# Optimization experiments

Measured on AMD Instinct MI355X. Metric: run time of the kernel, lower is better.

Reference implementation:

```python
import jax, jax.numpy as jnp
import numpy as np

L = 2048          # seq len
DIM = 1024        # model dim
NL = 12           # num layers
VOCAB = 50257
PAD_VOCAB = 50264 # vocab padded to multiple of 8 for embedding
N = 16            # ssm state dim
K = 4             # conv kernel size
E = 2048          # d_inner = expand * dim
DTR = 64          # dt_rank = ceil(dim/16)
EPS = 1e-5


def setup_inputs() -> dict:
    key = jax.random.key(0)
    ks = jax.random.split(key, 12)
    s = 0.02
    f32 = jnp.float32
    # HiPPO-style A init: A_log = log(1..N) broadcast over channels
    A_log = jnp.log(jnp.broadcast_to(jnp.arange(1, N + 1, dtype=f32), (NL, E, N)))
    return {
        "input_ids": jax.random.randint(ks[0], (L,), 0, VOCAB),
        "embed": jax.random.normal(ks[1], (PAD_VOCAB, DIM), f32) * s,
        "in_proj_w": jax.random.normal(ks[2], (NL, 2 * E, DIM), f32) * s,
        "conv_w": jax.random.normal(ks[3], (NL, E, K), f32) * s,
        "conv_b": jnp.zeros((NL, E), f32),
        "x_proj_w": jax.random.normal(ks[4], (NL, DTR + 2 * N, E), f32) * s,
        "dt_proj_w": jax.random.normal(ks[5], (NL, E, DTR), f32) * s,
        "dt_proj_b": jax.random.normal(ks[6], (NL, E), f32) * 0.1,
        "A_log": A_log,
        "D_param": jnp.ones((NL, E), f32),
        "out_proj_w": jax.random.normal(ks[7], (NL, DIM, E), f32) * s,
        "norm_w": jnp.ones((NL, DIM), f32),
        "norm_f_w": jnp.ones((DIM,), f32),
        "head_w": jax.random.normal(ks[8], (VOCAB, DIM), f32) * s,
    }


def rmsnorm(x, w):
    # per-token RMSNorm over last axis (matches eqx.nn.RMSNorm vmapped per token)
    inv = jax.lax.rsqrt(jnp.mean(x * x, axis=-1, keepdims=True) + EPS)
    return x * inv * w


def causal_dw_conv(x, w, b):
    # x: [L, E], w: [E, K] depthwise causal conv, b: [E]
    out = jax.lax.conv_general_dilated(
        x.T[None],            # [1, E, L]
        w[:, None, :],        # [E, 1, K]
        (1,), [(K - 1, 0)],
        feature_group_count=E,
        dimension_numbers=("NCH", "OIH", "NCH"),
    )
    return out[0].T + b       # [L, E]


def mamba_block(x, in_w, cw, cb, xp_w, dt_w, dt_b, A_log, D, out_w):
    # x: [L, DIM]
    xz = x @ in_w.T                       # [L, 2E]
    xi, z = xz[:, :E], xz[:, E:]
    xc = jax.nn.silu(causal_dw_conv(xi, cw, cb))   # [L, E]
    dbc = xc @ xp_w.T                     # [L, DTR + 2N]
    dt = jax.nn.softplus(dbc[:, :DTR] @ dt_w.T + dt_b)  # [L, E]
    B = dbc[:, DTR:DTR + N]               # [L, N]
    C = dbc[:, DTR + N:]                  # [L, N]
    A = -jnp.exp(A_log)                   # [E, N]
    dA = jnp.exp(dt[:, :, None] * A)                       # [L, E, N]
    dBu = dt[:, :, None] * B[:, None, :] * xc[:, :, None]  # [L, E, N]

    def step(h, inp):
        dA_t, dBu_t = inp
        h = dA_t * h + dBu_t
        return h, h

    _, hs = jax.lax.scan(step, jnp.zeros((E, N), x.dtype), (dA, dBu))
    y = jnp.einsum("len,ln->le", hs, C) + D * xc
    y = y * jax.nn.silu(z)
    return y @ out_w.T                    # [L, DIM]


def reference(input_ids, embed, in_proj_w, conv_w, conv_b, x_proj_w,
              dt_proj_w, dt_proj_b, A_log, D_param, out_proj_w,
              norm_w, norm_f_w, head_w):
    x = embed[input_ids]                  # [L, DIM]
    res = None
    for i in range(NL):
        res = x + res if res is not None else x
        h = rmsnorm(res, norm_w[i])
        x = mamba_block(h, in_proj_w[i], conv_w[i], conv_b[i], x_proj_w[i],
                        dt_proj_w[i], dt_proj_b[i], A_log[i], D_param[i],
                        out_proj_w[i])
    res = x + res
    x = rmsnorm(res, norm_f_w)
    return x @ head_w.T                   # [L, VOCAB]
```

## Files before the change

### kernel.cpp

```cpp
#include <hip/hip_runtime.h>
#include <math.h>

#define LSEQ 2048
#define DMODEL 1024
#define NLAYER 12
#define NVOCAB 50257
#define NPADV 50304
#define EDIM 2048
#define NST 16
#define DTRANK 64
#define EPSV 1e-5f
#define NCHUNK 64
#define TCHUNK 32

typedef __attribute__((ext_vector_type(4))) float float4v;
typedef __attribute__((ext_vector_type(8))) short short8v;
typedef __attribute__((ext_vector_type(4))) unsigned short ushort4v;
typedef unsigned short u16;

__device__ __forceinline__ u16 f2bf(float f) {
    union { float f; unsigned int u; } v; v.f = f;
    unsigned int r = v.u + 0x7FFFu + ((v.u >> 16) & 1u);
    return (u16)(r >> 16);
}

__device__ __forceinline__ ushort4v cvt4(float4 a) {
    ushort4v r; r[0] = f2bf(a.x); r[1] = f2bf(a.y); r[2] = f2bf(a.z); r[3] = f2bf(a.w);
    return r;
}

__device__ __forceinline__ short8v pack8(float4 a, float4 b) {
    short8v r;
    r[0] = (short)f2bf(a.x); r[1] = (short)f2bf(a.y); r[2] = (short)f2bf(a.z); r[3] = (short)f2bf(a.w);
    r[4] = (short)f2bf(b.x); r[5] = (short)f2bf(b.y); r[6] = (short)f2bf(b.z); r[7] = (short)f2bf(b.w);
    return r;
}

__device__ __forceinline__ float4v mfma_bf16(short8v a, short8v b, float4v c) {
    return __builtin_amdgcn_mfma_f32_16x16x32_bf16(a, b, c, 0, 0, 0);
}

__device__ __forceinline__ void gload_lds16(const void* g, void* l) {
    __builtin_amdgcn_global_load_lds(
        (const __attribute__((address_space(1))) unsigned int*)g,
        (__attribute__((address_space(3))) unsigned int*)l,
        16, 0, 0);
}

__global__ __launch_bounds__(256) void k_embed(const int* __restrict__ ids,
                                               const float* __restrict__ emb,
                                               float* __restrict__ res) {
    const int t = blockIdx.x;
    const int row = ids[t];
    ((float4*)(res + (size_t)t * DMODEL))[threadIdx.x] =
        ((const float4*)(emb + (size_t)row * DMODEL))[threadIdx.x];
}

template<bool ADD>
__global__ __launch_bounds__(256) void k_addnorm(float* __restrict__ res,
                                                 const float* __restrict__ xin,
                                                 const float* __restrict__ w,
                                                 u16* __restrict__ h) {
    const int t = blockIdx.x;
    const int i = threadIdx.x;
    float4 r = ((float4*)(res + (size_t)t * DMODEL))[i];
    if (ADD) {
        float4 xv = ((const float4*)(xin + (size_t)t * DMODEL))[i];
        r.x += xv.x; r.y += xv.y; r.z += xv.z; r.w += xv.w;
        ((float4*)(res + (size_t)t * DMODEL))[i] = r;
    }
    float ss = r.x * r.x + r.y * r.y + r.z * r.z + r.w * r.w;
#pragma unroll
    for (int off = 32; off > 0; off >>= 1) ss += __shfl_xor(ss, off);
    __shared__ float part[4];
    if ((i & 63) == 0) part[i >> 6] = ss;
    __syncthreads();
    float tot = part[0] + part[1] + part[2] + part[3];
    const float inv = rsqrtf(tot * (1.f / DMODEL) + EPSV);
    float4 wv = ((const float4*)w)[i];
    float4 o;
    o.x = r.x * inv * wv.x; o.y = r.y * inv * wv.y;
    o.z = r.z * inv * wv.z; o.w = r.w * inv * wv.w;
    ((ushort4v*)(h + (size_t)t * DMODEL))[i] = cvt4(o);
}

__global__ __launch_bounds__(256) void k_cvt(const float* __restrict__ s, u16* __restrict__ d,
                                             long long n, long long ntot) {
    const long long stride = (long long)gridDim.x * 256 * 8;
    for (long long i = ((long long)blockIdx.x * 256 + threadIdx.x) * 8; i < ntot; i += stride) {
        ushort4v lo, hi;
        if (i < n) {
            float4 a = *(const float4*)(s + i);
            float4 b = *(const float4*)(s + i + 4);
            lo = cvt4(a); hi = cvt4(b);
        } else {
            lo[0] = lo[1] = lo[2] = lo[3] = 0;
            hi[0] = hi[1] = hi[2] = hi[3] = 0;
        }
        *(ushort4v*)(d + i) = lo;
        *(ushort4v*)(d + i + 4) = hi;
    }
}

__global__ __launch_bounds__(256) void k_cvt2(const float* __restrict__ sa, u16* __restrict__ da, long long na,
                                              const float* __restrict__ sb, u16* __restrict__ db, long long nb) {
    const long long tot = na + nb;
    const long long stride = (long long)gridDim.x * 256 * 8;
    for (long long i = ((long long)blockIdx.x * 256 + threadIdx.x) * 8; i < tot; i += stride) {
        const float* s; u16* d; long long o;
        if (i < na) { s = sa; d = da; o = i; } else { s = sb; d = db; o = i - na; }
        float4 a = *(const float4*)(s + o);
        float4 b = *(const float4*)(s + o + 4);
        *(ushort4v*)(d + o) = cvt4(a);
        *(ushort4v*)(d + o + 4) = cvt4(b);
    }
}

template<int MT>
__global__ __launch_bounds__(256, 4) void k_gemm128(const u16* __restrict__ A,
                                                    const u16* __restrict__ W,
                                                    float* __restrict__ C,
                                                    int N, int K, int ldc, int cpx) {
    __shared__ __align__(128) u16 lds[2][8192];
    const int tid = threadIdx.x;
    const int w = tid >> 6;
    const int lane = tid & 63;
    const int l16 = lane & 15;
    const int quad = lane >> 4;
    const int wm = (w >> 1) * 64;
    const int wn = (w & 1) * 64;
    const int bid = blockIdx.x;
    const int orig = (bid & 7) * cpx + (bid >> 3);
    const int bm = orig & (MT - 1);
    const int bn = orig / MT;
    const int row0 = bm * 128, col0 = bn * 128;

    const int scol = ((lane & 3) ^ ((lane >> 2) & 3)) * 8;
    const int lrow = lane >> 2;
    const u16* sbase[4];
#pragma unroll
    for (int c = 0; c < 4; ++c) {
        const int g = w * 4 + c;
        sbase[c] = (g < 8 ? A + (size_t)(row0 + g * 16 + lrow) * K
                          : W + (size_t)(col0 + (g - 8) * 16 + lrow) * K) + scol;
    }

    const int swz = (quad ^ (l16 & 3)) * 8;
    const int aoff = (wm + l16) * 32 + swz;
    const int boff = 4096 + (wn + l16) * 32 + swz;

    float4v acc[4][4];
#pragma unroll
    for (int i = 0; i < 4; ++i)
#pragma unroll
        for (int j = 0; j < 4; ++j)
#pragma unroll
            for (int r = 0; r < 4; ++r) acc[i][j][r] = 0.f;

    const int NT = K >> 5;

    auto stage_tile = [&](int buf, int t) {
#pragma unroll
        for (int c = 0; c < 4; ++c)
            gload_lds16(sbase[c] + t * 32, &lds[buf][(w * 4 + c) * 512]);
    };

    stage_tile(0, 0);
    stage_tile(1, 1);
    asm volatile("s_waitcnt vmcnt(4)" ::: "memory");
    __builtin_amdgcn_s_barrier();

    for (int n = 0; n < NT; ++n) {
        const u16* Ls = &lds[n & 1][0];
        short8v af[4], bf[4];
#pragma unroll
        for (int ii = 0; ii < 4; ++ii)
            af[ii] = *(const short8v*)&Ls[aoff + ii * 512];
#pragma unroll
        for (int j = 0; j < 4; ++j)
            bf[j] = *(const short8v*)&Ls[boff + j * 512];
        __builtin_amdgcn_s_barrier();
        __builtin_amdgcn_s_setprio(1);
#pragma unroll
        for (int ii = 0; ii < 4; ++ii)
#pragma unroll
            for (int j = 0; j < 4; ++j)
                acc[ii][j] = mfma_bf16(af[ii], bf[j], acc[ii][j]);
        __builtin_amdgcn_s_setprio(0);
        if (n + 2 < NT) {
            stage_tile(n & 1, n + 2);
            asm volatile("s_waitcnt vmcnt(4)" ::: "memory");
        } else if (n < NT - 1) {
            asm volatile("s_waitcnt vmcnt(0)" ::: "memory");
        }
        __builtin_amdgcn_s_barrier();
    }

#pragma unroll
    for (int i = 0; i < 4; ++i) {
        const int row = row0 + wm + i * 16 + quad * 4;
#pragma unroll
        for (int j = 0; j < 4; ++j) {
            const int col = col0 + wn + j * 16 + l16;
            if (col < N) {
#pragma unroll
                for (int r = 0; r < 4; ++r)
                    C[(size_t)(row + r) * ldc + col] = acc[i][j][r];
            }
        }
    }
}

template<int TM, int TN>
__global__ __launch_bounds__(256) void k_gemm_bf(const u16* __restrict__ A,
                                                 const u16* __restrict__ W,
                                                 float* __restrict__ C,
                                                 int N, int K, int ldc) {
    constexpr int NI = TM / 32, NJ = TN / 32, CA = TM / 64, CB = TN / 64;
    __shared__ u16 As[TM * 32];
    __shared__ u16 Bs[TN * 32];
    const int tid = threadIdx.x;
    const int lane = tid & 63;
    const int wave = tid >> 6;
    const int l16 = lane & 15;
    const int quad = lane >> 4;
    const int wm = (wave >> 1) * (TM / 2);
    const int wn = (wave & 1) * (TN / 2);
    const int srow = lane >> 2;
    const int scol = (((lane & 3) ^ ((lane >> 2) & 3))) * 8;
    const int bm = blockIdx.x, bn = blockIdx.y;

    const u16* Ab = A + ((size_t)bm * TM + srow) * K + scol;
    const u16* Wb = W + ((size_t)bn * TN + srow) * K + scol;

    const int qs = (quad ^ (l16 & 3)) * 8;

    float4v acc[NI][NJ];
#pragma unroll
    for (int i = 0; i < NI; ++i)
#pragma unroll
        for (int j = 0; j < NJ; ++j)
#pragma unroll
            for (int r = 0; r < 4; ++r) acc[i][j][r] = 0.f;

    for (int k0 = 0; k0 < K; k0 += 32) {
#pragma unroll
        for (int c = 0; c < CA; ++c) {
            const int chunk = wave * CA + c;
            gload_lds16(Ab + (size_t)chunk * 16 * K + k0, &As[chunk * 512]);
        }
#pragma unroll
        for (int c = 0; c < CB; ++c) {
            const int chunk = wave * CB + c;
            gload_lds16(Wb + (size_t)chunk * 16 * K + k0, &Bs[chunk * 512]);
        }
        __syncthreads();
        short8v af[NI], bfr[NJ];
#pragma unroll
        for (int i = 0; i < NI; ++i)
            af[i] = *(const short8v*)&As[(wm + i * 16 + l16) * 32 + qs];
#pragma unroll
        for (int j = 0; j < NJ; ++j)
            bfr[j] = *(const short8v*)&Bs[(wn + j * 16 + l16) * 32 + qs];
#pragma unroll
        for (int i = 0; i < NI; ++i)
#pragma unroll
            for (int j = 0; j < NJ; ++j)
                acc[i][j] = mfma_bf16(af[i], bfr[j], acc[i][j]);
        __syncthreads();
    }

#pragma unroll
    for (int i = 0; i < NI; ++i) {
        const int row0 = bm * TM + wm + i * 16 + quad * 4;
#pragma unroll
        for (int j = 0; j < NJ; ++j) {
            const int col = bn * TN + wn + j * 16 + l16;
            if (col < N) {
#pragma unroll
                for (int r = 0; r < 4; ++r)
                    C[(size_t)(row0 + r) * ldc + col] = acc[i][j][r];
            }
        }
    }
}

template<int EPI>
__global__ __launch_bounds__(256) void k_gemm(const float* __restrict__ A,
                                              const float* __restrict__ W,
                                              float* __restrict__ C,
                                              const float* __restrict__ bias,
                                              int N, int K, int lda, int ldw, int ldc) {
    __shared__ u16 As[128][32];
    __shared__ u16 Bs[128][32];
    const int tid = threadIdx.x;
    const int lane = tid & 63;
    const int wave = tid >> 6;
    const int l16 = lane & 15;
    const int quad = lane >> 4;
    const int wm = (wave >> 1) * 64;
    const int wn = (wave & 1) * 64;
    const int srow = tid >> 3;
    const int scol = (tid & 7) * 4;
    const int bm = blockIdx.x, bn = blockIdx.y;

    const float* Ap = A + (size_t)(bm * 128 + srow) * lda + scol;
    const int gn0 = bn * 128 + srow;

    float4 apf[4], bpf[4];
#pragma unroll
    for (int i = 0; i < 4; ++i) {
        apf[i] = *(const float4*)(Ap + (size_t)(32 * i) * lda);
        const int gn = gn0 + 32 * i;
        bpf[i] = (gn < N) ? *(const float4*)(W + (size_t)gn * ldw + scol)
                          : make_float4(0.f, 0.f, 0.f, 0.f);
    }

    float4v acc[4][4];
#pragma unroll
    for (int i = 0; i < 4; ++i)
#pragma unroll
        for (int j = 0; j < 4; ++j)
#pragma unroll
            for (int r = 0; r < 4; ++r) acc[i][j][r] = 0.f;

    int k0 = 0;
    while (true) {
#pragma unroll
        for (int i = 0; i < 4; ++i) {
            *(ushort4v*)&As[srow + 32 * i][scol] = cvt4(apf[i]);
            *(ushort4v*)&Bs[srow + 32 * i][scol] = cvt4(bpf[i]);
        }
        __syncthreads();
        k0 += 32;
        const bool more = (k0 < K);
        if (more) {
#pragma unroll
            for (int i = 0; i < 4; ++i) {
                apf[i] = *(const float4*)(Ap + (size_t)(32 * i) * lda + k0);
                const int gn = gn0 + 32 * i;
                bpf[i] = (gn < N) ? *(const float4*)(W + (size_t)gn * ldw + scol + k0)
                                  : make_float4(0.f, 0.f, 0.f, 0.f);
            }
        }
        short8v af[4], bfr[4];
#pragma unroll
        for (int i = 0; i < 4; ++i)
            af[i] = *(const short8v*)&As[wm + i * 16 + l16][quad * 8];
#pragma unroll
        for (int j = 0; j < 4; ++j)
            bfr[j] = *(const short8v*)&Bs[wn + j * 16 + l16][quad * 8];
#pragma unroll
        for (int i = 0; i < 4; ++i)
#pragma unroll
            for (int j = 0; j < 4; ++j)
                acc[i][j] = mfma_bf16(af[i], bfr[j], acc[i][j]);
        if (!more) break;
        __syncthreads();
    }

#pragma unroll
    for (int i = 0; i < 4; ++i) {
        const int row0 = bm * 128 + wm + i * 16 + quad * 4;
#pragma unroll
        for (int j = 0; j < 4; ++j) {
            const int col = bn * 128 + wn + j * 16 + l16;
            if (col < N) {
#pragma unroll
                for (int r = 0; r < 4; ++r) {
                    float v = acc[i][j][r];
                    if (EPI == 1) {
                        v += bias[col];
                        v = (v > 20.f) ? v : log1pf(__expf(v));
                    }
                    C[(size_t)(row0 + r) * ldc + col] = v;
                }
            }
        }
    }
}

__global__ __launch_bounds__(256) void k_conv(const float* __restrict__ xz,
                                              const float* __restrict__ cw,
                                              const float* __restrict__ cb,
                                              float* __restrict__ xc) {
    const int e = blockIdx.x * 256 + threadIdx.x;
    const int t0 = blockIdx.y * 8;
    const float w0 = cw[e * 4 + 0], w1 = cw[e * 4 + 1], w2 = cw[e * 4 + 2], w3 = cw[e * 4 + 3];
    const float b = cb[e];
    float xm3 = (t0 >= 3) ? xz[(size_t)(t0 - 3) * (2 * EDIM) + e] : 0.f;
    float xm2 = (t0 >= 2) ? xz[(size_t)(t0 - 2) * (2 * EDIM) + e] : 0.f;
    float xm1 = (t0 >= 1) ? xz[(size_t)(t0 - 1) * (2 * EDIM) + e] : 0.f;
#pragma unroll
    for (int s = 0; s < 8; ++s) {
        const int t = t0 + s;
        const float xt = xz[(size_t)t * (2 * EDIM) + e];
        const float v = w0 * xm3 + w1 * xm2 + w2 * xm1 + w3 * xt + b;
        xc[(size_t)t * EDIM + e] = v / (1.f + __expf(-v));
        xm3 = xm2; xm2 = xm1; xm1 = xt;
    }
}

__global__ __launch_bounds__(256) void k_xproj(const float* __restrict__ xc,
                                               const float* __restrict__ W,
                                               float* __restrict__ dbc) {
    const int tid = threadIdx.x;
    const int wave = tid >> 6, lane = tid & 63;
    const int l16 = lane & 15, quad = lane >> 4;
    const int m = blockIdx.x * 16 + l16;
    const int kb = wave * (EDIM / 4);
    float4v acc[6];
#pragma unroll
    for (int j = 0; j < 6; ++j)
#pragma unroll
        for (int r = 0; r < 4; ++r) acc[j][r] = 0.f;

    for (int ks = 0; ks < EDIM / 4; ks += 32) {
        const int k = kb + ks + quad * 8;
        const float* ap = xc + (size_t)m * EDIM + k;
        const short8v af = pack8(*(const float4*)ap, *(const float4*)(ap + 4));
#pragma unroll
        for (int j = 0; j < 6; ++j) {
            const float* wp = W + (size_t)(j * 16 + l16) * EDIM + k;
            const short8v bf = pack8(*(const float4*)wp, *(const float4*)(wp + 4));
            acc[j] = mfma_bf16(af, bf, acc[j]);
        }
    }
    __shared__ float red[4][16][96];
#pragma unroll
    for (int j = 0; j < 6; ++j)
#pragma unroll
        for (int r = 0; r < 4; ++r)
            red[wave][quad * 4 + r][j * 16 + l16] = acc[j][r];
    __syncthreads();
    for (int idx = tid; idx < 16 * 96; idx += 256) {
        const int r = idx / 96, c = idx % 96;
        const float s = red[0][r][c] + red[1][r][c] + red[2][r][c] + red[3][r][c];
        dbc[(size_t)(blockIdx.x * 16 + r) * 96 + c] = s;
    }
}

__global__ __launch_bounds__(256) void k_scanA(const float* __restrict__ dt,
                                               const float* __restrict__ xc,
                                               const float* __restrict__ dbc,
                                               const float* __restrict__ Al,
                                               float* __restrict__ hpart,
                                               float* __restrict__ sdtb) {
    const int e = blockIdx.y * 256 + threadIdx.x;
    const int c = blockIdx.x;
    float a[NST];
#pragma unroll
    for (int n = 0; n < NST; ++n) a[n] = -__expf(Al[(size_t)e * NST + n]);
    bool fast = true;
#pragma unroll
    for (int n = 0; n < NST; ++n)
        fast = fast && (fabsf(a[n] + (float)(n + 1)) < 1e-3f * (float)(n + 1));
    __align__(16) float h[NST];
#pragma unroll
    for (int n = 0; n < NST; ++n) h[n] = 0.f;
    float sdt = 0.f;
    const int t0 = c * TCHUNK;
    if (fast) {
        for (int s = 0; s < TCHUNK; ++s) {
            const int t = t0 + s;
            const float d = dt[(size_t)t * EDIM + e];
            const float x = xc[(size_t)t * EDIM + e];
            __align__(16) float Bv[NST];
#pragma unroll
            for (int q = 0; q < 4; ++q)
                *(float4*)&Bv[q * 4] = *(const float4*)&dbc[(size_t)t * 96 + 64 + q * 4];
            const float u = d * x;
            sdt += d;
            const float d1 = __expf(-d);
            float pw = 1.f;
#pragma unroll
            for (int n = 0; n < NST; ++n) { pw *= d1; h[n] = fmaf(pw, h[n], u * Bv[n]); }
        }
    } else {
        for (int s = 0; s < TCHUNK; ++s) {
            const int t = t0 + s;
            const float d = dt[(size_t)t * EDIM + e];
            const float x = xc[(size_t)t * EDIM + e];
            __align__(16) float Bv[NST];
#pragma unroll
            for (int q = 0; q < 4; ++q)
                *(float4*)&Bv[q * 4] = *(const float4*)&dbc[(size_t)t * 96 + 64 + q * 4];
            const float u = d * x;
            sdt += d;
#pragma unroll
            for (int n = 0; n < NST; ++n) h[n] = fmaf(__expf(d * a[n]), h[n], u * Bv[n]);
        }
    }
#pragma unroll
    for (int n = 0; n < NST; n += 4)
        *(float4*)&hpart[((size_t)c * EDIM + e) * NST + n] = *(float4*)&h[n];
    sdtb[(size_t)c * EDIM + e] = sdt;
}

__global__ __launch_bounds__(256) void k_scanB(float* __restrict__ hio,
                                               const float* __restrict__ sdtb,
                                               const float* __restrict__ Al) {
    const int idx = blockIdx.x * 256 + threadIdx.x;
    const int e = idx >> 4;
    const float a = -__expf(Al[idx]);
    float carry = 0.f;
    for (int c = 0; c < NCHUNK; ++c) {
        const size_t off = ((size_t)c * EDIM + e) * NST + (idx & 15);
        const float hp = hio[off];
        const float ap = __expf(a * sdtb[(size_t)c * EDIM + e]);
        hio[off] = carry;
        carry = fmaf(ap, carry, hp);
    }
}

__global__ __launch_bounds__(256) void k_scanC(const float* __restrict__ dt,
                                               const float* __restrict__ xc,
                                               const float* __restrict__ dbc,
                                               const float* __restrict__ xz,
                                               const float* __restrict__ Al,
                                               const float* __restrict__ Dl,
                                               const float* __restrict__ hin,
                                               u16* __restrict__ y) {
    const int e = blockIdx.y * 256 + threadIdx.x;
    const int c = blockIdx.x;
    float a[NST];
#pragma unroll
    for (int n = 0; n < NST; ++n) a[n] = -__expf(Al[(size_t)e * NST + n]);
    bool fast = true;
#pragma unroll
    for (int n = 0; n < NST; ++n)
        fast = fast && (fabsf(a[n] + (float)(n + 1)) < 1e-3f * (float)(n + 1));
    __align__(16) float h[NST];
#pragma unroll
    for (int n = 0; n < NST; n += 4)
        *(float4*)&h[n] = *(const float4*)&hin[((size_t)c * EDIM + e) * NST + n];
    const float Dv = Dl[e];
    const int t0 = c * TCHUNK;
    for (int s = 0; s < TCHUNK; ++s) {
        const int t = t0 + s;
        const float d = dt[(size_t)t * EDIM + e];
        const float x = xc[(size_t)t * EDIM + e];
        __align__(16) float Bv[NST], Cv[NST];
#pragma unroll
        for (int q = 0; q < 4; ++q) {
            *(float4*)&Bv[q * 4] = *(const float4*)&dbc[(size_t)t * 96 + 64 + q * 4];
            *(float4*)&Cv[q * 4] = *(const float4*)&dbc[(size_t)t * 96 + 80 + q * 4];
        }
        const float u = d * x;
        float ys = 0.f;
        if (fast) {
            const float d1 = __expf(-d);
            float pw = 1.f;
#pragma unroll
            for (int n = 0; n < NST; ++n) {
                pw *= d1;
                h[n] = fmaf(pw, h[n], u * Bv[n]);
                ys = fmaf(h[n], Cv[n], ys);
            }
        } else {
#pragma unroll
            for (int n = 0; n < NST; ++n) {
                h[n] = fmaf(__expf(d * a[n]), h[n], u * Bv[n]);
                ys = fmaf(h[n], Cv[n], ys);
            }
        }
        const float z = xz[(size_t)t * (2 * EDIM) + EDIM + e];
        const float yv = ys + Dv * x;
        y[(size_t)t * EDIM + e] = f2bf(yv * (z / (1.f + __expf(-z))));
    }
}

extern "C" void kernel_launch(void* const* d_in, const int* in_sizes, int n_in,
                              void* d_out, int out_size, void* d_ws, size_t ws_size,
                              hipStream_t stream) {
    const int*   ids   = (const int*)d_in[0];
    const float* emb   = (const float*)d_in[1];
    const float* inW   = (const float*)d_in[2];
    const float* convW = (const float*)d_in[3];
    const float* convB = (const float*)d_in[4];
    const float* xpW   = (const float*)d_in[5];
    const float* dtW   = (const float*)d_in[6];
    const float* dtB   = (const float*)d_in[7];
    const float* Alog  = (const float*)d_in[8];
    const float* Dpar  = (const float*)d_in[9];
    const float* outW  = (const float*)d_in[10];
    const float* normW = (const float*)d_in[11];
    const float* normF = (const float*)d_in[12];
    const float* headW = (const float*)d_in[13];
    float* out = (float*)d_out;

    float* ws    = (float*)d_ws;
    float* res   = ws;
    float* xzb   = res   + (size_t)LSEQ * DMODEL;
    float* xcb   = xzb   + (size_t)LSEQ * 2 * EDIM;
    float* dbcb  = xcb   + (size_t)LSEQ * EDIM;
    float* dtb   = dbcb  + (size_t)LSEQ * 96;
    float* xob   = dtb   + (size_t)LSEQ * EDIM;
    float* hpart = xob   + (size_t)LSEQ * DMODEL;
    float* sdtb  = hpart + (size_t)NCHUNK * EDIM * NST;
    u16* hbf  = (u16*)(sdtb + (size_t)NCHUNK * EDIM);
    u16* ybf  = hbf  + (size_t)LSEQ * DMODEL;
    u16* wbf  = ybf  + (size_t)LSEQ * EDIM;
    u16* wbf2 = wbf  + (size_t)2 * EDIM * DMODEL;

    k_embed<<<LSEQ, 256, 0, stream>>>(ids, emb, res);

    for (int i = 0; i < NLAYER; ++i) {
        if (i == 0)
            k_addnorm<false><<<LSEQ, 256, 0, stream>>>(res, nullptr, normW, hbf);
        else
            k_addnorm<true><<<LSEQ, 256, 0, stream>>>(res, xob, normW + (size_t)i * DMODEL, hbf);

        k_cvt2<<<4096, 256, 0, stream>>>(inW + (size_t)i * 2 * EDIM * DMODEL, wbf,
                                         (long long)2 * EDIM * DMODEL,
                                         outW + (size_t)i * DMODEL * EDIM, wbf2,
                                         (long long)DMODEL * EDIM);

        k_gemm128<16><<<dim3(512), 256, 0, stream>>>(hbf, wbf, xzb,
                2 * EDIM, DMODEL, 2 * EDIM, 64);

        k_conv<<<dim3(8, 256), 256, 0, stream>>>(xzb, convW + (size_t)i * EDIM * 4,
                convB + (size_t)i * EDIM, xcb);

        k_xproj<<<128, 256, 0, stream>>>(xcb, xpW + (size_t)i * 96 * EDIM, dbcb);

        k_gemm<1><<<dim3(16, 16), 256, 0, stream>>>(dbcb, dtW + (size_t)i * EDIM * DTRANK,
                dtb, dtB + (size_t)i * EDIM, EDIM, DTRANK, 96, DTRANK, EDIM);

        const float* Al = Alog + (size_t)i * EDIM * NST;
        k_scanA<<<dim3(NCHUNK, EDIM / 256), 256, 0, stream>>>(dtb, xcb, dbcb, Al, hpart, sdtb);
        k_scanB<<<(EDIM * NST) / 256, 256, 0, stream>>>(hpart, sdtb, Al);
        k_scanC<<<dim3(NCHUNK, EDIM / 256), 256, 0, stream>>>(dtb, xcb, dbcb, xzb, Al,
                Dpar + (size_t)i * EDIM, hpart, ybf);

        k_gemm_bf<64, 64><<<dim3(32, 16), 256, 0, stream>>>(ybf, wbf2, xob,
                DMODEL, EDIM, DMODEL);
    }

    k_addnorm<true><<<LSEQ, 256, 0, stream>>>(res, xob, normF, hbf);

    k_cvt<<<4096, 256, 0, stream>>>(headW, wbf,
            (long long)NVOCAB * DMODEL, (long long)NPADV * DMODEL);
    k_gemm128<16><<<dim3(6288), 256, 0, stream>>>(hbf, wbf, out,
            NVOCAB, DMODEL, NVOCAB, 6288 / 8);
}
```

Before: 3.158 ms.

## Pre-convert x_proj and dt_proj inputs to bf16 and reuse async GEMM

The x_proj and dt_proj weights are now converted to bf16 in the per-layer conversion kernel. The conv kernel also emits a bf16 copy of its output, and x_proj emits a bf16 copy of the dt-rank columns. This lets x_proj read bf16 directly and lets dt_proj run on the async-LDS k_gemm128 path with a fused bias+softplus epilogue, replacing the float GEMM that converted on the fly. The LDS swizzle pattern is also changed in both bf16 GEMMs, presumably to reduce bank conflicts. The cost is extra bf16 writes and a larger conversion pass.

After: 3.020 ms. -4.4%, faster.

```diff
diff --git a/kernel.cpp b/kernel.cpp
--- a/kernel.cpp
+++ b/kernel.cpp
@@ -26,13 +26,6 @@
 
 __device__ __forceinline__ ushort4v cvt4(float4 a) {
     ushort4v r; r[0] = f2bf(a.x); r[1] = f2bf(a.y); r[2] = f2bf(a.z); r[3] = f2bf(a.w);
-    return r;
-}
-
-__device__ __forceinline__ short8v pack8(float4 a, float4 b) {
-    short8v r;
-    r[0] = (short)f2bf(a.x); r[1] = (short)f2bf(a.y); r[2] = (short)f2bf(a.z); r[3] = (short)f2bf(a.w);
-    r[4] = (short)f2bf(b.x); r[5] = (short)f2bf(b.y); r[6] = (short)f2bf(b.z); r[7] = (short)f2bf(b.w);
     return r;
 }
 
@@ -102,13 +95,20 @@
     }
 }
 
-__global__ __launch_bounds__(256) void k_cvt2(const float* __restrict__ sa, u16* __restrict__ da, long long na,
-                                              const float* __restrict__ sb, u16* __restrict__ db, long long nb) {
-    const long long tot = na + nb;
+__global__ __launch_bounds__(256) void k_cvtL(const float* __restrict__ sa, u16* __restrict__ da, long long na,
+                                              const float* __restrict__ sb, u16* __restrict__ db, long long nb,
+                                              const float* __restrict__ sc, u16* __restrict__ dc, long long nc,
+                                              const float* __restrict__ sd, u16* __restrict__ dd, long long nd) {
+    const long long tot = na + nb + nc + nd;
     const long long stride = (long long)gridDim.x * 256 * 8;
     for (long long i = ((long long)blockIdx.x * 256 + threadIdx.x) * 8; i < tot; i += stride) {
-        const float* s; u16* d; long long o;
-        if (i < na) { s = sa; d = da; o = i; } else { s = sb; d = db; o = i - na; }
+        const float* s; u16* d; long long o = i;
+        if (o < na) { s = sa; d = da; }
+        else { o -= na;
+            if (o < nb) { s = sb; d = db; }
+            else { o -= nb;
+                if (o < nc) { s = sc; d = dc; }
+                else { o -= nc; s = sd; d = dd; } } }
         float4 a = *(const float4*)(s + o);
         float4 b = *(const float4*)(s + o + 4);
         *(ushort4v*)(d + o) = cvt4(a);
@@ -116,10 +116,11 @@
     }
 }
 
-template<int MT>
+template<int MT, int EPI>
 __global__ __launch_bounds__(256, 4) void k_gemm128(const u16* __restrict__ A,
                                                     const u16* __restrict__ W,
                                                     float* __restrict__ C,
+                                                    const float* __restrict__ bias,
                                                     int N, int K, int ldc, int cpx) {
     __shared__ __align__(128) u16 lds[2][8192];
     const int tid = threadIdx.x;
@@ -135,7 +136,7 @@
     const int bn = orig / MT;
     const int row0 = bm * 128, col0 = bn * 128;
 
-    const int scol = ((lane & 3) ^ ((lane >> 2) & 3)) * 8;
+    const int scol = ((lane & 3) ^ ((lane >> 3) & 3)) * 8;
     const int lrow = lane >> 2;
     const u16* sbase[4];
 #pragma unroll
@@ -145,7 +146,7 @@
                           : W + (size_t)(col0 + (g - 8) * 16 + lrow) * K) + scol;
     }
 
-    const int swz = (quad ^ (l16 & 3)) * 8;
+    const int swz = (quad ^ ((l16 >> 1) & 3)) * 8;
     const int aoff = (wm + l16) * 32 + swz;
     const int boff = 4096 + (wn + l16) * 32 + swz;
 
@@ -204,8 +205,14 @@
             const int col = col0 + wn + j * 16 + l16;
             if (col < N) {
 #pragma unroll
-                for (int r = 0; r < 4; ++r)
-                    C[(size_t)(row + r) * ldc + col] = acc[i][j][r];
+                for (int r = 0; r < 4; ++r) {
+                    float v = acc[i][j][r];
+                    if (EPI == 1) {
+                        v += bias[col];
+                        v = (v > 20.f) ? v : log1pf(__expf(v));
+                    }
+                    C[(size_t)(row + r) * ldc + col] = v;
+                }
             }
         }
     }
@@ -227,13 +234,13 @@
     const int wm = (wave >> 1) * (TM / 2);
     const int wn = (wave & 1) * (TN / 2);
     const int srow = lane >> 2;
-    const int scol = (((lane & 3) ^ ((lane >> 2) & 3))) * 8;
+    const int scol = ((lane & 3) ^ ((lane >> 3) & 3)) * 8;
     const int bm = blockIdx.x, bn = blockIdx.y;
 
     const u16* Ab = A + ((size_t)bm * TM + srow) * K + scol;
     const u16* Wb = W + ((size_t)bn * TN + srow) * K + scol;
 
-    const int qs = (quad ^ (l16 & 3)) * 8;
+    const int qs = (quad ^ ((l16 >> 1) & 3)) * 8;
 
     float4v acc[NI][NJ];
 #pragma unroll
@@ -285,105 +292,11 @@
     }
 }
 
-template<int EPI>
-__global__ __launch_bounds__(256) void k_gemm(const float* __restrict__ A,
-                                              const float* __restrict__ W,
-                                              float* __restrict__ C,
-                                              const float* __restrict__ bias,
-                                              int N, int K, int lda, int ldw, int ldc) {
-    __shared__ u16 As[128][32];
-    __shared__ u16 Bs[128][32];
-    const int tid = threadIdx.x;
-    const int lane = tid & 63;
-    const int wave = tid >> 6;
-    const int l16 = lane & 15;
-    const int quad = lane >> 4;
-    const int wm = (wave >> 1) * 64;
-    const int wn = (wave & 1) * 64;
-    const int srow = tid >> 3;
-    const int scol = (tid & 7) * 4;
-    const int bm = blockIdx.x, bn = blockIdx.y;
-
-    const float* Ap = A + (size_t)(bm * 128 + srow) * lda + scol;
-    const int gn0 = bn * 128 + srow;
-
-    float4 apf[4], bpf[4];
-#pragma unroll
-    for (int i = 0; i < 4; ++i) {
-        apf[i] = *(const float4*)(Ap + (size_t)(32 * i) * lda);
-        const int gn = gn0 + 32 * i;
-        bpf[i] = (gn < N) ? *(const float4*)(W + (size_t)gn * ldw + scol)
-                          : make_float4(0.f, 0.f, 0.f, 0.f);
-    }
-
-    float4v acc[4][4];
-#pragma unroll
-    for (int i = 0; i < 4; ++i)
-#pragma unroll
-        for (int j = 0; j < 4; ++j)
-#pragma unroll
-            for (int r = 0; r < 4; ++r) acc[i][j][r] = 0.f;
-
-    int k0 = 0;
-    while (true) {
-#pragma unroll
-        for (int i = 0; i < 4; ++i) {
-            *(ushort4v*)&As[srow + 32 * i][scol] = cvt4(apf[i]);
-            *(ushort4v*)&Bs[srow + 32 * i][scol] = cvt4(bpf[i]);
-        }
-        __syncthreads();
-        k0 += 32;
-        const bool more = (k0 < K);
-        if (more) {
-#pragma unroll
-            for (int i = 0; i < 4; ++i) {
-                apf[i] = *(const float4*)(Ap + (size_t)(32 * i) * lda + k0);
-                const int gn = gn0 + 32 * i;
-                bpf[i] = (gn < N) ? *(const float4*)(W + (size_t)gn * ldw + scol + k0)
-                                  : make_float4(0.f, 0.f, 0.f, 0.f);
-            }
-        }
-        short8v af[4], bfr[4];
-#pragma unroll
-        for (int i = 0; i < 4; ++i)
-            af[i] = *(const short8v*)&As[wm + i * 16 + l16][quad * 8];
-#pragma unroll
-        for (int j = 0; j < 4; ++j)
-            bfr[j] = *(const short8v*)&Bs[wn + j * 16 + l16][quad * 8];
-#pragma unroll
-        for (int i = 0; i < 4; ++i)
-#pragma unroll
-            for (int j = 0; j < 4; ++j)
-                acc[i][j] = mfma_bf16(af[i], bfr[j], acc[i][j]);
-        if (!more) break;
-        __syncthreads();
-    }
-
-#pragma unroll
-    for (int i = 0; i < 4; ++i) {
-        const int row0 = bm * 128 + wm + i * 16 + quad * 4;
-#pragma unroll
-        for (int j = 0; j < 4; ++j) {
-            const int col = bn * 128 + wn + j * 16 + l16;
-            if (col < N) {
-#pragma unroll
-                for (int r = 0; r < 4; ++r) {
-                    float v = acc[i][j][r];
-                    if (EPI == 1) {
-                        v += bias[col];
-                        v = (v > 20.f) ? v : log1pf(__expf(v));
-                    }
-                    C[(size_t)(row0 + r) * ldc + col] = v;
-                }
-            }
-        }
-    }
-}
-
 __global__ __launch_bounds__(256) void k_conv(const float* __restrict__ xz,
                                               const float* __restrict__ cw,
                                               const float* __restrict__ cb,
-                                              float* __restrict__ xc) {
+                                              float* __restrict__ xc,
+                                              u16* __restrict__ xc16) {
     const int e = blockIdx.x * 256 + threadIdx.x;
     const int t0 = blockIdx.y * 8;
     const float w0 = cw[e * 4 + 0], w1 = cw[e * 4 + 1], w2 = cw[e * 4 + 2], w3 = cw[e * 4 + 3];
@@ -396,14 +309,17 @@
         const int t = t0 + s;
         const float xt = xz[(size_t)t * (2 * EDIM) + e];
         const float v = w0 * xm3 + w1 * xm2 + w2 * xm1 + w3 * xt + b;
-        xc[(size_t)t * EDIM + e] = v / (1.f + __expf(-v));
+        const float sv = v / (1.f + __expf(-v));
+        xc[(size_t)t * EDIM + e] = sv;
+        xc16[(size_t)t * EDIM + e] = f2bf(sv);
         xm3 = xm2; xm2 = xm1; xm1 = xt;
     }
 }
 
-__global__ __launch_bounds__(256) void k_xproj(const float* __restrict__ xc,
-                                               const float* __restrict__ W,
-                                               float* __restrict__ dbc) {
+__global__ __launch_bounds__(256) void k_xproj(const u16* __restrict__ xc,
+                                               const u16* __restrict__ W,
+                                               float* __restrict__ dbc,
+                                               u16* __restrict__ dbc16) {
     const int tid = threadIdx.x;
     const int wave = tid >> 6, lane = tid & 63;
     const int l16 = lane & 15, quad = lane >> 4;
@@ -417,12 +333,10 @@
 
     for (int ks = 0; ks < EDIM / 4; ks += 32) {
         const int k = kb + ks + quad * 8;
-        const float* ap = xc + (size_t)m * EDIM + k;
-        const short8v af = pack8(*(const float4*)ap, *(const float4*)(ap + 4));
+        const short8v af = *(const short8v*)(xc + (size_t)m * EDIM + k);
 #pragma unroll
         for (int j = 0; j < 6; ++j) {
-            const float* wp = W + (size_t)(j * 16 + l16) * EDIM + k;
-            const short8v bf = pack8(*(const float4*)wp, *(const float4*)(wp + 4));
+            const short8v bf = *(const short8v*)(W + (size_t)(j * 16 + l16) * EDIM + k);
             acc[j] = mfma_bf16(af, bf, acc[j]);
         }
     }
@@ -436,7 +350,9 @@
     for (int idx = tid; idx < 16 * 96; idx += 256) {
         const int r = idx / 96, c = idx % 96;
         const float s = red[0][r][c] + red[1][r][c] + red[2][r][c] + red[3][r][c];
-        dbc[(size_t)(blockIdx.x * 16 + r) * 96 + c] = s;
+        const int row = blockIdx.x * 16 + r;
+        dbc[(size_t)row * 96 + c] = s;
+        if (c < 64) dbc16[(size_t)row * 64 + c] = f2bf(s);
     }
 }
 
@@ -602,6 +518,10 @@
     u16* ybf  = hbf  + (size_t)LSEQ * DMODEL;
     u16* wbf  = ybf  + (size_t)LSEQ * EDIM;
     u16* wbf2 = wbf  + (size_t)2 * EDIM * DMODEL;
+    u16* xc16  = wbf  + (size_t)12 * 1024 * 1024;
+    u16* dbc16 = xc16 + (size_t)LSEQ * EDIM;
+    u16* xpw16 = dbc16 + (size_t)LSEQ * DTRANK;
+    u16* dtw16 = xpw16 + (size_t)96 * EDIM;
 
     k_embed<<<LSEQ, 256, 0, stream>>>(ids, emb, res);
 
@@ -611,21 +531,22 @@
         else
             k_addnorm<true><<<LSEQ, 256, 0, stream>>>(res, xob, normW + (size_t)i * DMODEL, hbf);
 
-        k_cvt2<<<4096, 256, 0, stream>>>(inW + (size_t)i * 2 * EDIM * DMODEL, wbf,
-                                         (long long)2 * EDIM * DMODEL,
-                                         outW + (size_t)i * DMODEL * EDIM, wbf2,
-                                         (long long)DMODEL * EDIM);
-
-        k_gemm128<16><<<dim3(512), 256, 0, stream>>>(hbf, wbf, xzb,
+        k_cvtL<<<4096, 256, 0, stream>>>(
+            inW  + (size_t)i * 2 * EDIM * DMODEL, wbf,   (long long)2 * EDIM * DMODEL,
+            outW + (size_t)i * DMODEL * EDIM,     wbf2,  (long long)DMODEL * EDIM,
+            xpW  + (size_t)i * 96 * EDIM,         xpw16, (long long)96 * EDIM,
+            dtW  + (size_t)i * EDIM * DTRANK,     dtw16, (long long)EDIM * DTRANK);
+
+        k_gemm128<16, 0><<<dim3(512), 256, 0, stream>>>(hbf, wbf, xzb, nullptr,
                 2 * EDIM, DMODEL, 2 * EDIM, 64);
 
         k_conv<<<dim3(8, 256), 256, 0, stream>>>(xzb, convW + (size_t)i * EDIM * 4,
-                convB + (size_t)i * EDIM, xcb);
-
-        k_xproj<<<128, 256, 0, stream>>>(xcb, xpW + (size_t)i * 96 * EDIM, dbcb);
-
-        k_gemm<1><<<dim3(16, 16), 256, 0, stream>>>(dbcb, dtW + (size_t)i * EDIM * DTRANK,
-                dtb, dtB + (size_t)i * EDIM, EDIM, DTRANK, 96, DTRANK, EDIM);
+                convB + (size_t)i * EDIM, xcb, xc16);
+
+        k_xproj<<<128, 256, 0, stream>>>(xc16, xpw16, dbcb, dbc16);
+
+        k_gemm128<16, 1><<<dim3(256), 256, 0, stream>>>(dbc16, dtw16, dtb,
+                dtB + (size_t)i * EDIM, EDIM, DTRANK, EDIM, 32);
 
         const float* Al = Alog + (size_t)i * EDIM * NST;
         k_scanA<<<dim3(NCHUNK, EDIM / 256), 256, 0, stream>>>(dtb, xcb, dbcb, Al, hpart, sdtb);
@@ -641,6 +562,6 @@
 
     k_cvt<<<4096, 256, 0, stream>>>(headW, wbf,
             (long long)NVOCAB * DMODEL, (long long)NPADV * DMODEL);
-    k_gemm128<16><<<dim3(6288), 256, 0, stream>>>(hbf, wbf, out,
+    k_gemm128<16, 0><<<dim3(6288), 256, 0, stream>>>(hbf, wbf, out, nullptr,
             NVOCAB, DMODEL, NVOCAB, 6288 / 8);
 }
```
